# Performance work log

Hardware: AMD Instinct MI355X
Metric: run time of the kernel (lower is better)

Reference implementation:

```python
import jax, jax.numpy as jnp
import numpy as np


def setup_inputs() -> dict:
    key = jax.random.key(0)
    ks = jax.random.split(key, 8)
    B, Cin, Cattr, Cout, H, W = 8, 256, 256, 256, 64, 64
    x = jax.random.normal(ks[0], (B, Cin, H, W), dtype=jnp.float32)
    attr = jax.random.normal(ks[1], (B, Cattr, H, W), dtype=jnp.float32)
    # 1x1 conv weights stored as [out, in] (kernel_size=1 squeezed)
    sq = 1.0 / np.sqrt(Cin)
    sa = 1.0 / np.sqrt(Cattr)
    Wq = jax.random.uniform(ks[2], (Cout, Cin), jnp.float32, -sq, sq)
    bq = jax.random.uniform(ks[3], (Cout,), jnp.float32, -sq, sq)
    Wk = jax.random.uniform(ks[4], (Cout, Cattr), jnp.float32, -sa, sa)
    bk = jax.random.uniform(ks[5], (Cout,), jnp.float32, -sa, sa)
    Wv = jax.random.uniform(ks[6], (Cout, Cattr), jnp.float32, -sa, sa)
    bv = jax.random.uniform(ks[7], (Cout,), jnp.float32, -sa, sa)
    return {"x": x, "attr": attr, "Wq": Wq, "bq": bq, "Wk": Wk, "bk": bk, "Wv": Wv, "bv": bv}


def reference(x, attr, Wq, bq, Wk, bk, Wv, bv):
    B, Cin, H, W = x.shape
    # 1x1 convs == per-pixel linear projections
    q = jnp.einsum('bchw,oc->bohw', x, Wq) + bq[None, :, None, None]      # [B,C,H,W]
    k = jnp.einsum('bchw,oc->bohw', attr, Wk) + bk[None, :, None, None]
    v = jnp.einsum('bchw,oc->bohw', attr, Wv) + bv[None, :, None, None]
    C = q.shape[1]
    qf = q.reshape(B, C, H * W)   # [B,C,N]
    kf = k.reshape(B, C, H * W)
    vf = v.reshape(B, C, H * W)
    # attn[b,i,j] = sum_c q[b,c,i] * k[b,c,j]  -> softmax over j
    attn = jax.nn.softmax(jnp.einsum('bci,bcj->bij', qf, kf), axis=-1)    # [B,N,N]
    out = jnp.einsum('bcj,bij->bci', vf, attn)                            # [B,C,N]
    return out.reshape(B, C, H, W) + x
```

## Files before the change

### kernel.cpp

```cpp
#include <hip/hip_runtime.h>

typedef _Float16 f16;
typedef _Float16 f16x8 __attribute__((ext_vector_type(8)));
typedef _Float16 f16x4 __attribute__((ext_vector_type(4)));
typedef float f32x4 __attribute__((ext_vector_type(4)));
typedef float f32x16 __attribute__((ext_vector_type(16)));

#define LOG2E 1.44269504088896340736f
#define SOFF  36.0f
#define CDIM 256
#define NPIX 4096

__device__ __forceinline__ void gl2lds16(const f16* g, const f16* l) {
    __builtin_amdgcn_global_load_lds((const __attribute__((address_space(1))) unsigned int*)g,
                                     (__attribute__((address_space(3))) unsigned int*)l, 16, 0, 0);
}

__global__ void convert_w_kernel(const float* __restrict__ Wq, const float* __restrict__ Wk,
                                 const float* __restrict__ Wv,
                                 f16* __restrict__ WqF, f16* __restrict__ WkF,
                                 f16* __restrict__ WvF) {
    int t = blockIdx.x * 256 + threadIdx.x;
    int m = t >> 13;
    int g = t & 8191;
    int lane = g & 63;
    int ksct = g >> 6;
    int ks = ksct & 15, ct = ksct >> 4;
    int o = ct * 32 + (lane & 31);
    int cin0 = ks * 16 + (lane >> 5) * 8;
    const float* W = (m == 0) ? Wq : ((m == 1) ? Wk : Wv);
    f16* WF = (m == 0) ? WqF : ((m == 1) ? WkF : WvF);
    const float scale = (m == 0) ? LOG2E : 1.0f;
    const float* src = W + (size_t)o * CDIM + cin0;
    f16x8 v;
#pragma unroll
    for (int e = 0; e < 8; ++e) v[e] = (f16)(src[e] * scale);
    *(f16x8*)(WF + (size_t)g * 8) = v;
}

__global__ __launch_bounds__(256, 2)
void proj_kernel(const float* __restrict__ x, const float* __restrict__ attr,
                 const f16* __restrict__ WqF, const float* __restrict__ bq,
                 const f16* __restrict__ WkF, const float* __restrict__ bk,
                 const f16* __restrict__ WvF, const float* __restrict__ bv,
                 f16* __restrict__ qT, f16* __restrict__ kT, f16* __restrict__ vW) {
    __shared__ __align__(16) f16 Xs[64 * 256];
    __shared__ __align__(16) f16 As[64 * 256];
    __shared__ __align__(16) f16 Ostage[4][1024];

    const int b  = blockIdx.x & 7;
    const int i0 = (blockIdx.x >> 3) * 64;
    const int t  = threadIdx.x;
    const int w = t >> 6, lane = t & 63, l31 = lane & 31, hi = lane >> 5;
    const int xu  = (l31 >> 1) & 15;
    const int hib = (hi ^ (l31 & 1)) * 8;

    {
        const int i  = t & 63;
        const int cb = t >> 6;
        const float* xb = x    + (size_t)b * CDIM * NPIX + i0 + i;
        const float* ab = attr + (size_t)b * CDIM * NPIX + i0 + i;
#pragma unroll 2
        for (int rep = 0; rep < 8; ++rep) {
            int chunk = cb * 8 + rep;
            const float* xs = xb + (size_t)(chunk * 8) * NPIX;
            const float* as_ = ab + (size_t)(chunk * 8) * NPIX;
            f16x8 xv, av;
#pragma unroll
            for (int e = 0; e < 8; ++e) {
                xv[e] = (f16)xs[(size_t)e * NPIX];
                av[e] = (f16)as_[(size_t)e * NPIX];
            }
            int phys = chunk ^ (i & 31);
            *(f16x8*)(Xs + i * 256 + phys * 8) = xv;
            *(f16x8*)(As + i * 256 + phys * 8) = av;
        }
    }
    __syncthreads();

#pragma unroll 1
    for (int k = 0; k < 12; ++k) {
        const int tt = w + 4 * k;
        const int kind = tt >> 4;
        const int rr = tt & 15;
        const int ct = rr >> 1;
        const int half = rr & 1;

        const f16* WF = (kind == 0) ? WqF : ((kind == 1) ? WkF : WvF);
        const f16* Bs = (kind == 0) ? Xs : As;
        const float* bias = (kind == 0) ? bq : ((kind == 1) ? bk : bv);
        const float bscale = (kind == 0) ? LOG2E : 1.0f;

        const f16* ap = WF + (size_t)(ct * 16) * 512 + (size_t)lane * 8;
        const f16* bp = Bs + (half * 32 + l31) * 256 + hib;

        f32x16 acc;
#pragma unroll
        for (int r = 0; r < 16; ++r) acc[r] = 0.0f;
#pragma unroll
        for (int ks = 0; ks < 16; ++ks) {
            f16x8 afr = *(const f16x8*)(ap + ks * 512);
            f16x8 bfr = *(const f16x8*)(bp + ((ks ^ xu) << 4));
            acc = __builtin_amdgcn_mfma_f32_32x32x16_f16(afr, bfr, acc, 0, 0, 0);
        }

        f16* st = Ostage[w];
        if (kind < 2) {
#pragma unroll
            for (int g = 0; g < 4; ++g) {
                f32x4 bb = *(const f32x4*)(bias + ct * 32 + 4 * hi + 8 * g);
                f16x4 pk;
#pragma unroll
                for (int e = 0; e < 4; ++e) pk[e] = (f16)(acc[4 * g + e] + bb[e] * bscale);
                *(f16x4*)(st + l31 * 32 + 4 * hi + 8 * g) = pk;
            }
            f16* dst = ((kind == 0) ? qT : kT)
                       + ((size_t)b * NPIX + i0 + half * 32) * CDIM + ct * 32;
#pragma unroll
            for (int d = 0; d < 2; ++d) {
                int row = d * 16 + (lane >> 2);
                int c8  = (lane & 3) * 8;
                f16x8 v = *(const f16x8*)(st + row * 32 + c8);
                *(f16x8*)(dst + (size_t)row * CDIM + c8) = v;
            }
        } else {
#pragma unroll
            for (int g = 0; g < 4; ++g) {
                f32x4 bb = *(const f32x4*)(bias + ct * 32 + 4 * hi + 8 * g);
#pragma unroll
                for (int e = 0; e < 4; ++e) {
                    int c31 = 4 * hi + 8 * g + e;
                    st[c31 * 32 + l31] = (f16)(acc[4 * g + e] + bb[e]);
                }
            }
            const int j0 = i0 + half * 32;
            f16* dstb = vW + (size_t)b * CDIM * NPIX + (size_t)(ct * 32) * NPIX + j0;
#pragma unroll
            for (int d = 0; d < 2; ++d) {
                int chunk = d * 64 + lane;
                int c31 = chunk >> 2, jch = chunk & 3;
                *(f16x8*)(dstb + (size_t)c31 * NPIX + jch * 8) =
                    *(const f16x8*)(st + chunk * 8);
            }
        }
    }
}

__global__ __launch_bounds__(512, 2)
void attn_kernel(const f16* __restrict__ qT, const f16* __restrict__ kT,
                 const f16* __restrict__ vW, const float* __restrict__ x,
                 float* __restrict__ out) {
    extern __shared__ unsigned char smem[];

    const int b    = blockIdx.x & 7;
    const int i0   = (blockIdx.x >> 3) * 128;
    const int t    = threadIdx.x;
    const int w    = t >> 6;
    const int lane = t & 63;
    const int l31  = lane & 31;
    const int hi   = lane >> 5;
    const int iw   = (w & 3) * 32;
    const int jh   = (w >> 2) * 32;
    const int jh8  = (w >> 2) * 4;
    const int ig   = i0 + iw + l31;

    f16x8 qf[16];
    {
        const f16* qp = qT + ((size_t)b * NPIX + ig) * CDIM + hi * 8;
#pragma unroll
        for (int ks = 0; ks < 16; ++ks) qf[ks] = *(const f16x8*)(qp + ks * 16);
    }

    const int xu  = (l31 >> 1) & 15;
    const int kbase = (jh + l31) * 256 + (hi ^ (l31 & 1)) * 8;
    int vp2o[2];
    {
        int vbase = 16384 + (l31 >> 2) * 256 + (l31 & 3) * 64;
#pragma unroll
        for (int kj = 0; kj < 2; ++kj)
            vp2o[kj] = vbase + (((jh8 + 2 * kj + hi) ^ (l31 & 7))) * 8;
    }

    f32x16 acc[8];
#pragma unroll
    for (int ct = 0; ct < 8; ++ct)
#pragma unroll
        for (int r = 0; r < 16; ++r) acc[ct][r] = 0.0f;
    float lrun = 0.0f;

    const f16* kb = kT + (size_t)b * NPIX * CDIM;
    const f16* vb = vW + (size_t)b * CDIM * NPIX;
    f16* lds0 = (f16*)smem;
    const int wub = (t & ~63) * 8;

    {
#pragma unroll
        for (int rep = 0; rep < 4; ++rep) {
            int slot = t + rep * 512;
            int krow = slot >> 5, kpc = slot & 31;
            gl2lds16(kb + (size_t)krow * CDIM + ((kpc ^ (krow & 31)) * 8),
                     lds0 + wub + rep * 4096);
            int R = slot >> 5, pv = slot & 31;
            int vc = 4 * R + (pv >> 3);
            int vjc = (pv & 7) ^ (vc & 7);
            gl2lds16(vb + (size_t)vc * NPIX + vjc * 8,
                     lds0 + 16384 + wub + rep * 4096);
        }
    }

    union Q4 { f16x4 h; unsigned int u[2]; };
    union B8 { f16x8 h; unsigned int u[4]; };

#pragma unroll 1
    for (int jt = 0; jt < 64; ++jt) {
        const int p = jt & 1;
        __syncthreads();

        if (jt < 63) {
            const int j0n = (jt + 1) * 64;
            f16* dstb = lds0 + (p ^ 1) * 32768;
#pragma unroll
            for (int rep = 0; rep < 4; ++rep) {
                int slot = t + rep * 512;
                int krow = slot >> 5, kpc = slot & 31;
                gl2lds16(kb + (size_t)(j0n + krow) * CDIM + ((kpc ^ (krow & 31)) * 8),
                         dstb + wub + rep * 4096);
                int R = slot >> 5, pv = slot & 31;
                int vc = 4 * R + (pv >> 3);
                int vjc = (pv & 7) ^ (vc & 7);
                gl2lds16(vb + (size_t)vc * NPIX + j0n + vjc * 8,
                         dstb + 16384 + wub + rep * 4096);
            }
        }

        const f16* L = lds0 + p * 32768;

        f32x16 s;
#pragma unroll
        for (int r = 0; r < 16; ++r) s[r] = -SOFF;
        __builtin_amdgcn_s_setprio(1);
#pragma unroll
        for (int ks = 0; ks < 16; ++ks)
            s = __builtin_amdgcn_mfma_f32_32x32x16_f16(
                *(const f16x8*)(L + kbase + ((ks ^ xu) << 4)), qf[ks], s, 0, 0, 0);
        __builtin_amdgcn_s_setprio(0);

        Q4 ownq[4];
        float rtot = 0.0f;
#pragma unroll
        for (int g = 0; g < 4; ++g) {
            float p0 = __builtin_amdgcn_exp2f(s[4 * g + 0]);
            float p1 = __builtin_amdgcn_exp2f(s[4 * g + 1]);
            float p2 = __builtin_amdgcn_exp2f(s[4 * g + 2]);
            float p3 = __builtin_amdgcn_exp2f(s[4 * g + 3]);
            rtot += (p0 + p1) + (p2 + p3);
            ownq[g].h[0] = (f16)p0; ownq[g].h[1] = (f16)p1;
            ownq[g].h[2] = (f16)p2; ownq[g].h[3] = (f16)p3;
        }
        lrun += rtot;

        f16x8 pb[2];
#pragma unroll
        for (int kj = 0; kj < 2; ++kj) {
            int sidx = 2 * kj + 1 - hi;
            int oidx = 2 * kj + hi;
            unsigned int s0 = ownq[sidx].u[0], s1 = ownq[sidx].u[1];
            unsigned int r0 = (unsigned int)__shfl_xor((int)s0, 32);
            unsigned int r1 = (unsigned int)__shfl_xor((int)s1, 32);
            B8 bb;
            bb.u[0] = hi ? r0 : ownq[oidx].u[0];
            bb.u[1] = hi ? r1 : ownq[oidx].u[1];
            bb.u[2] = hi ? ownq[oidx].u[0] : r0;
            bb.u[3] = hi ? ownq[oidx].u[1] : r1;
            pb[kj] = bb.h;
        }

        __builtin_amdgcn_s_setprio(1);
#pragma unroll
        for (int ct = 0; ct < 8; ++ct) {
            acc[ct] = __builtin_amdgcn_mfma_f32_32x32x16_f16(
                *(const f16x8*)(L + vp2o[0] + ct * 2048), pb[0], acc[ct], 0, 0, 0);
            acc[ct] = __builtin_amdgcn_mfma_f32_32x32x16_f16(
                *(const f16x8*)(L + vp2o[1] + ct * 2048), pb[1], acc[ct], 0, 0, 0);
        }
        __builtin_amdgcn_s_setprio(0);
    }

    float lsum = lrun + __shfl_xor(lrun, 32);
    __syncthreads();
    float* Obuf = (float*)smem;
    float* Ls   = (float*)(smem + 131072);
    if (w >= 4) {
        float* ob = Obuf + (w - 4) * 8192;
#pragma unroll
        for (int ct = 0; ct < 8; ++ct)
#pragma unroll
            for (int r = 0; r < 16; ++r) {
                int c = ct * 32 + (r & 3) + 8 * (r >> 2) + 4 * hi;
                ob[c * 32 + l31] = acc[ct][r];
            }
        if (hi == 0) Ls[(w - 4) * 32 + l31] = lsum;
    }
    __syncthreads();
    if (w < 4) {
        const float ltot = lsum + Ls[w * 32 + l31];
        const float invl = 1.0f / ltot;
        const float* po = Obuf + w * 8192;
        const float* xb = x + (size_t)b * CDIM * NPIX + i0 + iw;
        float* og = out + (size_t)b * CDIM * NPIX + i0 + iw;
#pragma unroll
        for (int ct = 0; ct < 8; ++ct)
#pragma unroll
            for (int r = 0; r < 16; ++r) {
                int c = ct * 32 + (r & 3) + 8 * (r >> 2) + 4 * hi;
                size_t off = (size_t)c * NPIX + l31;
                og[off] = (acc[ct][r] + po[c * 32 + l31]) * invl + xb[off];
            }
    }
}

extern "C" void kernel_launch(void* const* d_in, const int* in_sizes, int n_in,
                              void* d_out, int out_size, void* d_ws, size_t ws_size,
                              hipStream_t stream) {
    const float* x    = (const float*)d_in[0];
    const float* attr = (const float*)d_in[1];
    const float* Wq   = (const float*)d_in[2];
    const float* bq   = (const float*)d_in[3];
    const float* Wk   = (const float*)d_in[4];
    const float* bk   = (const float*)d_in[5];
    const float* Wv   = (const float*)d_in[6];
    const float* bv   = (const float*)d_in[7];
    float* out = (float*)d_out;

    char* ws = (char*)d_ws;
    const size_t qkv_bytes = (size_t)8 * NPIX * CDIM * sizeof(f16);
    f16* qT   = (f16*)ws;
    f16* kT   = (f16*)(ws + qkv_bytes);
    f16* vW   = (f16*)(ws + 2 * qkv_bytes);
    f16* WqF  = (f16*)(ws + 3 * qkv_bytes);
    f16* WkF  = WqF + 65536;
    f16* WvF  = WkF + 65536;

    (void)hipFuncSetAttribute((const void*)attn_kernel,
                              hipFuncAttributeMaxDynamicSharedMemorySize, 131584);

    convert_w_kernel<<<96, 256, 0, stream>>>(Wq, Wk, Wv, WqF, WkF, WvF);
    proj_kernel<<<512, 256, 0, stream>>>(x, attr, WqF, bq, WkF, bk, WvF, bv, qT, kT, vW);
    attn_kernel<<<256, 512, 131584, stream>>>(qT, kT, vW, x, out);
}
```

Measured before the change: 332.4 us.

## Double-buffer weight fragments in projection kernel and drop setprio in attention

The projection kernel now prefetches the next tile's 16 weight fragments from global memory into registers while computing the current tile, using two register buffers and a loop unrolled by two. The MFMA chain is also split into two independent accumulators (even and odd k-steps) that are summed at the end, which shortens the dependency chain. Separately, the s_setprio raises around the MFMA blocks in the attention kernel are removed. The double buffering adds about 64 VGPRs of live fragments, which may lower occupancy. Dropping the priority hints changes how waves interleave in the attention kernel, and that could help or hurt.

```diff
diff --git a/kernel.cpp b/kernel.cpp
--- a/kernel.cpp
+++ b/kernel.cpp
@@ -78,30 +78,37 @@
     }
     __syncthreads();
 
-#pragma unroll 1
-    for (int k = 0; k < 12; ++k) {
+    auto prefetch = [&](int k, f16x8* af) {
+        const int tt = w + 4 * k;
+        const int kind = tt >> 4;
+        const int ct = (tt & 15) >> 1;
+        const f16* WF = (kind == 0) ? WqF : ((kind == 1) ? WkF : WvF);
+        const f16* ap = WF + (size_t)(ct * 16) * 512 + (size_t)lane * 8;
+#pragma unroll
+        for (int ks = 0; ks < 16; ++ks) af[ks] = *(const f16x8*)(ap + ks * 512);
+    };
+
+    auto do_tile = [&](int k, const f16x8* af) {
         const int tt = w + 4 * k;
         const int kind = tt >> 4;
         const int rr = tt & 15;
         const int ct = rr >> 1;
         const int half = rr & 1;
 
-        const f16* WF = (kind == 0) ? WqF : ((kind == 1) ? WkF : WvF);
         const f16* Bs = (kind == 0) ? Xs : As;
         const float* bias = (kind == 0) ? bq : ((kind == 1) ? bk : bv);
         const float bscale = (kind == 0) ? LOG2E : 1.0f;
-
-        const f16* ap = WF + (size_t)(ct * 16) * 512 + (size_t)lane * 8;
         const f16* bp = Bs + (half * 32 + l31) * 256 + hib;
 
-        f32x16 acc;
-#pragma unroll
-        for (int r = 0; r < 16; ++r) acc[r] = 0.0f;
-#pragma unroll
-        for (int ks = 0; ks < 16; ++ks) {
-            f16x8 afr = *(const f16x8*)(ap + ks * 512);
-            f16x8 bfr = *(const f16x8*)(bp + ((ks ^ xu) << 4));
-            acc = __builtin_amdgcn_mfma_f32_32x32x16_f16(afr, bfr, acc, 0, 0, 0);
+        f32x16 ae, ao;
+#pragma unroll
+        for (int r = 0; r < 16; ++r) { ae[r] = 0.0f; ao[r] = 0.0f; }
+#pragma unroll
+        for (int h2 = 0; h2 < 8; ++h2) {
+            f16x8 b0 = *(const f16x8*)(bp + (((2 * h2) ^ xu) << 4));
+            f16x8 b1 = *(const f16x8*)(bp + (((2 * h2 + 1) ^ xu) << 4));
+            ae = __builtin_amdgcn_mfma_f32_32x32x16_f16(af[2 * h2], b0, ae, 0, 0, 0);
+            ao = __builtin_amdgcn_mfma_f32_32x32x16_f16(af[2 * h2 + 1], b1, ao, 0, 0, 0);
         }
 
         f16* st = Ostage[w];
@@ -111,7 +118,8 @@
                 f32x4 bb = *(const f32x4*)(bias + ct * 32 + 4 * hi + 8 * g);
                 f16x4 pk;
 #pragma unroll
-                for (int e = 0; e < 4; ++e) pk[e] = (f16)(acc[4 * g + e] + bb[e] * bscale);
+                for (int e = 0; e < 4; ++e)
+                    pk[e] = (f16)(ae[4 * g + e] + ao[4 * g + e] + bb[e] * bscale);
                 *(f16x4*)(st + l31 * 32 + 4 * hi + 8 * g) = pk;
             }
             f16* dst = ((kind == 0) ? qT : kT)
@@ -130,7 +138,7 @@
 #pragma unroll
                 for (int e = 0; e < 4; ++e) {
                     int c31 = 4 * hi + 8 * g + e;
-                    st[c31 * 32 + l31] = (f16)(acc[4 * g + e] + bb[e]);
+                    st[c31 * 32 + l31] = (f16)(ae[4 * g + e] + ao[4 * g + e] + bb[e]);
                 }
             }
             const int j0 = i0 + half * 32;
@@ -143,6 +151,16 @@
                     *(const f16x8*)(st + chunk * 8);
             }
         }
+    };
+
+    f16x8 afA[16], afB[16];
+    prefetch(0, afA);
+#pragma unroll 1
+    for (int k = 0; k < 12; k += 2) {
+        prefetch(k + 1, afB);
+        do_tile(k, afA);
+        if (k < 10) prefetch(k + 2, afA);
+        do_tile(k + 1, afB);
     }
 }
 
@@ -238,12 +256,10 @@
         f32x16 s;
 #pragma unroll
         for (int r = 0; r < 16; ++r) s[r] = -SOFF;
-        __builtin_amdgcn_s_setprio(1);
 #pragma unroll
         for (int ks = 0; ks < 16; ++ks)
             s = __builtin_amdgcn_mfma_f32_32x32x16_f16(
                 *(const f16x8*)(L + kbase + ((ks ^ xu) << 4)), qf[ks], s, 0, 0, 0);
-        __builtin_amdgcn_s_setprio(0);
 
         Q4 ownq[4];
         float rtot = 0.0f;
@@ -275,7 +291,6 @@
             pb[kj] = bb.h;
         }
 
-        __builtin_amdgcn_s_setprio(1);
 #pragma unroll
         for (int ct = 0; ct < 8; ++ct) {
             acc[ct] = __builtin_amdgcn_mfma_f32_32x32x16_f16(
@@ -283,7 +298,6 @@
             acc[ct] = __builtin_amdgcn_mfma_f32_32x32x16_f16(
                 *(const f16x8*)(L + vp2o[1] + ct * 2048), pb[1], acc[ct], 0, 0, 0);
         }
-        __builtin_amdgcn_s_setprio(0);
     }
 
     float lsum = lrun + __shfl_xor(lrun, 32);
```

After: 341.7 us. +2.8%, slower.
